# Kernel optimization log

Hardware: AMD Instinct MI355X
Metric: run time of the kernel (lower is better)

## Reference

```python
import jax, jax.numpy as jnp
import numpy as np

B, T, K, H = 32, 128, 16, 4   # batch, agents, in_dim, num_heads
A = 2                          # out_dim (action dim)
H1 = H2 = 256
LOG_STD_MIN, LOG_STD_MAX = -20.0, 2.0


def _linear_params(key, out_dim, in_dim, uniform_w=None):
    k1, k2 = jax.random.split(key)
    if uniform_w is not None:
        w = jax.random.uniform(k1, (out_dim, in_dim), minval=-uniform_w, maxval=uniform_w)
        b = jax.random.uniform(k2, (out_dim,), minval=-uniform_w, maxval=uniform_w)
    else:
        bound = 1.0 / np.sqrt(in_dim)
        w = jax.random.uniform(k1, (out_dim, in_dim), minval=-bound, maxval=bound)
        b = jax.random.uniform(k2, (out_dim,), minval=-bound, maxval=bound)
    return w.astype(jnp.float32), b.astype(jnp.float32)


def setup_inputs() -> dict:
    key = jax.random.key(0)
    ks = jax.random.split(key, 10)
    state = jax.random.normal(ks[0], (B, T, K), dtype=jnp.float32)
    eps = jax.random.normal(ks[1], (B, T, A), dtype=jnp.float32)
    Wq, bq = _linear_params(ks[2], K * H, K)
    Wk, bk = _linear_params(ks[3], K * H, K)
    Wv, bv = _linear_params(ks[4], K * H, K)
    W1, b1 = _linear_params(ks[5], H1, K * H + K)
    W2, b2 = _linear_params(ks[6], H2, H1)
    Wmu, bmu = _linear_params(ks[7], A, H2, uniform_w=0.003)
    Wls, bls = _linear_params(ks[8], A, H2, uniform_w=0.003)
    return {"state": state, "eps": eps, "Wq": Wq, "bq": bq, "Wk": Wk, "bk": bk,
            "Wv": Wv, "bv": bv, "W1": W1, "b1": b1, "W2": W2, "b2": b2,
            "Wmu": Wmu, "bmu": bmu, "Wls": Wls, "bls": bls}


def reference(state, eps, Wq, bq, Wk, bk, Wv, bv, W1, b1, W2, b2, Wmu, bmu, Wls, bls):
    b, t, k = state.shape
    h = H
    # rel[b,i,j] = state[b,j] - state[b,i]
    rel = state[:, None, :, :] - state[:, :, None, :]          # (b,t,t,k)
    q = jax.nn.relu(state @ Wq.T + bq).reshape(b, t, h, k)     # (b,t,h,k)
    q = q.transpose(0, 2, 1, 3)                                # (b,h,t,k)
    Kt = jax.nn.relu(rel @ Wk.T + bk).reshape(b, t, t, h, k)   # (b,i,j,h,k)
    V = jax.nn.relu(rel @ Wv.T + bv).reshape(b, t, t, h, k)
    # scores over pairwise keys vs per-agent query; softmax over j (dim=2 in torch)
    s = jnp.einsum('bijhk,bhik->bhij', Kt, q) / jnp.sqrt(jnp.float32(k))
    w = jax.nn.softmax(s, axis=3)                              # softmax over j
    x = jnp.einsum('bhij,bijhk->bhik', w, V)                   # (b,h,t,k)
    x = x.transpose(0, 2, 1, 3).reshape(b, t, h * k)           # (b,t,h*k)
    x = jnp.concatenate([x, state], axis=-1)                   # (b,t,h*k+k)
    x = jax.nn.relu(x @ W1.T + b1)
    x = jax.nn.relu(x @ W2.T + b2)
    mu = jnp.tanh(x @ Wmu.T + bmu)
    log_std = jnp.tanh(x @ Wls.T + bls)
    log_std = LOG_STD_MIN + 0.5 * (LOG_STD_MAX - LOG_STD_MIN) * (log_std + 1.0)
    std = jnp.exp(log_std)
    z = mu + std * eps                                         # rsample
    action = jnp.tanh(z)
    # Normal log_prob with (z-mu)/std == eps, minus tanh correction
    log_prob = (-0.5 * eps * eps - log_std - 0.5 * jnp.log(2.0 * jnp.pi)) \
               - jnp.log(1.0 - action * action + 1e-7)
    log_prob = jnp.sum(log_prob, axis=-1, keepdims=True)
    return action, log_prob
```

## Files before the change

### kernel.cpp

```cpp
#include <hip/hip_runtime.h>
#include <math.h>

#define NB 32
#define NT 128
#define KD 16

#define QG_OFF   0u
#define PKH_OFF  1048576u
#define PVT_OFF  1572864u
#define W1P_OFF  2097152u
#define W2P_OFF  2146304u

typedef float f32x4 __attribute__((ext_vector_type(4)));
typedef short bf16x8 __attribute__((ext_vector_type(8)));
typedef __fp16 f16x2 __attribute__((ext_vector_type(2)));
union U4B8 { uint4 u; bf16x8 h; };
union U4H8 { uint4 u; f16x2 h[4]; };

#define L_PK 0
#define L_PV 18432
#define L_P  35840
#define L_X  44544
#define L_TOT 47872
#define L_H1 0
#define L_H2 8448

__device__ __forceinline__ unsigned short bf16rne(float f) {
    unsigned u = __float_as_uint(f);
    return (unsigned short)((u + 0x7fffu + ((u >> 16) & 1u)) >> 16);
}
__device__ __forceinline__ void unpack8(uint4 u, float* f) {
    f[0] = __uint_as_float(u.x << 16); f[1] = __uint_as_float(u.x & 0xffff0000u);
    f[2] = __uint_as_float(u.y << 16); f[3] = __uint_as_float(u.y & 0xffff0000u);
    f[4] = __uint_as_float(u.z << 16); f[5] = __uint_as_float(u.z & 0xffff0000u);
    f[6] = __uint_as_float(u.w << 16); f[7] = __uint_as_float(u.w & 0xffff0000u);
}
__device__ __forceinline__ f16x2 pkmax(f16x2 a, f16x2 b) {
    f16x2 d;
    asm("v_pk_max_f16 %0, %1, %2" : "=v"(d) : "v"(a), "v"(b));
    return d;
}
#if __has_builtin(__builtin_amdgcn_fdot2)
#define FDOT2(a, b, c) __builtin_amdgcn_fdot2((a), (b), (c), false)
#else
#define FDOT2(a, b, c) ((c) + (float)(a)[0] * (float)(b)[0] + (float)(a)[1] * (float)(b)[1])
#endif

__global__ __launch_bounds__(256) void prep_kernel(
    const float* __restrict__ state,
    const float* __restrict__ Wq, const float* __restrict__ bq,
    const float* __restrict__ Wk, const float* __restrict__ Wv,
    const float* __restrict__ W1, const float* __restrict__ W2,
    char* __restrict__ wsb)
{
    const int blk = blockIdx.x, tid = threadIdx.x;
    float* Qg = (float*)(wsb + QG_OFF);
    unsigned short* PkH = (unsigned short*)(wsb + PKH_OFF);
    unsigned short* PvT = (unsigned short*)(wsb + PVT_OFF);

    if (blk < 128) {
        __shared__ float Wl[3][64][17];
        __shared__ float Sl[32][17];
        const int b = blk >> 2, r0 = (blk & 3) * 32;
        for (int idx = tid; idx < 1024; idx += 256) {
            int o = idx >> 4, m = idx & 15;
            Wl[0][o][m] = Wq[idx];
            Wl[1][o][m] = Wk[idx];
            Wl[2][o][m] = Wv[idx];
        }
        for (int idx = tid; idx < 512; idx += 256)
            Sl[idx >> 4][idx & 15] = state[(size_t)(b * NT + r0) * KD + idx];
        __syncthreads();
        const int o = tid & 63, rr = tid >> 6;
        float wqv[16], wkv[16], wvv[16];
        #pragma unroll
        for (int m = 0; m < 16; ++m) {
            wqv[m] = Wl[0][o][m]; wkv[m] = Wl[1][o][m]; wvv[m] = Wl[2][o][m];
        }
        const float bqo = bq[o];
        for (int r = rr; r < 32; r += 4) {
            float aq = bqo, ak = 0.f, av = 0.f;
            #pragma unroll
            for (int m = 0; m < 16; ++m) {
                float s = Sl[r][m];
                aq = fmaf(s, wqv[m], aq);
                ak = fmaf(s, wkv[m], ak);
                av = fmaf(s, wvv[m], av);
            }
            int row = b * NT + r0 + r;
            Qg[row * 64 + o] = fmaxf(aq, 0.f) * 0.25f;
            __fp16 hk = (__fp16)ak;
            PkH[(size_t)b * 8192 + (r0 + r) * 64 + o] = *(unsigned short*)&hk;
            __fp16 hv = (__fp16)av;
            PvT[(size_t)b * 8192 + o * NT + (r0 + r)] = *(unsigned short*)&hv;
        }
    } else if (blk < 140) {
        int fi = (blk - 128) * 256 + tid;
        int l = fi & 63, rest = fi >> 6;
        int t = rest & 15, ks = rest >> 4;
        int n = t * 16 + (l & 15);
        int kb = ks * 32 + (l >> 4) * 8;
        unsigned short v[8];
        #pragma unroll
        for (int j = 0; j < 8; ++j) {
            int k = kb + j;
            v[j] = (k < 80) ? bf16rne(W1[n * 80 + k]) : (unsigned short)0;
        }
        uint4 u;
        u.x = (unsigned)v[0] | ((unsigned)v[1] << 16);
        u.y = (unsigned)v[2] | ((unsigned)v[3] << 16);
        u.z = (unsigned)v[4] | ((unsigned)v[5] << 16);
        u.w = (unsigned)v[6] | ((unsigned)v[7] << 16);
        ((uint4*)(wsb + W1P_OFF))[fi] = u;
    } else {
        int fi = (blk - 140) * 256 + tid;
        int l = fi & 63, rest = fi >> 6;
        int t = rest & 15, ks = rest >> 4;
        int n = t * 16 + (l & 15);
        int kb = ks * 32 + (l >> 4) * 8;
        unsigned short v[8];
        #pragma unroll
        for (int j = 0; j < 8; ++j) v[j] = bf16rne(W2[n * 256 + kb + j]);
        uint4 u;
        u.x = (unsigned)v[0] | ((unsigned)v[1] << 16);
        u.y = (unsigned)v[2] | ((unsigned)v[3] << 16);
        u.z = (unsigned)v[4] | ((unsigned)v[5] << 16);
        u.w = (unsigned)v[6] | ((unsigned)v[7] << 16);
        ((uint4*)(wsb + W2P_OFF))[fi] = u;
    }
}

__global__ __launch_bounds__(512, 4) void actor_kernel(
    const float* __restrict__ state, const float* __restrict__ eps,
    const float* __restrict__ bkg, const float* __restrict__ bvg,
    const float* __restrict__ b1g, const float* __restrict__ b2g,
    const float* __restrict__ Wmu, const float* __restrict__ bmu,
    const float* __restrict__ Wls, const float* __restrict__ bls,
    const char* __restrict__ wsb, float* __restrict__ out)
{
    __shared__ __align__(16) char sm[L_TOT];

    const int tid = threadIdx.x, w = tid >> 6, lane = tid & 63;
    const int bid = blockIdx.x;
    const int b    = (bid & 7) * 4 + ((bid >> 3) >> 4);
    const int tile = (bid >> 3) & 15;
    const int iloc = tile * 8 + w;
    const int row  = b * NT + iloc;
    const int h = lane >> 4, s = lane & 15, h16 = h << 4;
    const int g = h, lr = s;
    const int t0 = 2 * w;
    const int n0 = w * 32 + lr, n1 = n0 + 16;

    const float* Qg = (const float*)(wsb + QG_OFF);

    {
        const uint4* srcK = (const uint4*)(wsb + PKH_OFF) + (size_t)b * 1024;
        #pragma unroll
        for (int it = 0; it < 2; ++it) {
            int idx = tid + it * 512;
            int r = idx >> 3, c = idx & 7;
            *(uint4*)(sm + L_PK + r * 144 + c * 16) = srcK[idx];
        }
        const uint4* srcV = (const uint4*)(wsb + PVT_OFF) + (size_t)b * 1024;
        #pragma unroll
        for (int it = 0; it < 2; ++it) {
            int idx = tid + it * 512;
            int o = idx >> 4, c = idx & 15;
            *(uint4*)(sm + L_PV + o * 272 + c * 16) = srcV[idx];
        }
        if (tid < 384) {
            int r = 8 + tid / 48, c2 = (tid % 48) * 2;
            *(unsigned*)((unsigned short*)(sm + L_X) + r * 104 + c2) = 0u;
        }
    }

    float qf[16], bkf[16];
    {
        const float4* qa  = (const float4*)(Qg + (size_t)row * 64 + h16);
        const float4* bk4 = (const float4*)(bkg + h16);
        #pragma unroll
        for (int q4 = 0; q4 < 4; ++q4) {
            float4 a = qa[q4], k4 = bk4[q4];
            qf[q4*4+0]=a.x; qf[q4*4+1]=a.y; qf[q4*4+2]=a.z; qf[q4*4+3]=a.w;
            bkf[q4*4+0]=k4.x; bkf[q4*4+1]=k4.y; bkf[q4*4+2]=k4.z; bkf[q4*4+3]=k4.w;
        }
    }
    const float bvo = bvg[lane];
    float stt = 0.f;
    if (tid < 128)
        stt = state[((size_t)b * NT + tile * 8 + (tid >> 4)) * KD + (tid & 15)];
    __syncthreads();

    f16x2 q8[8], mb8[8];
    float dotc;
    {
        U4H8 p0, p1;
        p0.u = *(const uint4*)(sm + L_PK + iloc * 144 + h * 32);
        p1.u = *(const uint4*)(sm + L_PK + iloc * 144 + h * 32 + 16);
        #pragma unroll
        for (int t = 0; t < 4; ++t) {
            q8[t]     = __builtin_amdgcn_cvt_pkrtz(qf[2*t],   qf[2*t+1]);
            q8[4 + t] = __builtin_amdgcn_cvt_pkrtz(qf[8+2*t], qf[8+2*t+1]);
            f16x2 b0 = __builtin_amdgcn_cvt_pkrtz(bkf[2*t],   bkf[2*t+1]);
            f16x2 b1 = __builtin_amdgcn_cvt_pkrtz(bkf[8+2*t], bkf[8+2*t+1]);
            mb8[t]     = p0.h[t] - b0;
            mb8[4 + t] = p1.h[t] - b1;
        }
        float d0 = 0.f, d1 = 0.f;
        #pragma unroll
        for (int t = 0; t < 4; ++t) {
            d0 = FDOT2(q8[t],     mb8[t],     d0);
            d1 = FDOT2(q8[4 + t], mb8[4 + t], d1);
        }
        dotc = -(d0 + d1);
    }

    float sc[8];
    #pragma unroll
    for (int jj = 0; jj < 8; ++jj) {
        const char* pr = sm + L_PK + (s + (jj << 4)) * 144 + h * 32;
        U4H8 v0, v1;
        v0.u = *(const uint4*)(pr);
        v1.u = *(const uint4*)(pr + 16);
        float aE = 0.f, aO = 0.f;
        #pragma unroll
        for (int t = 0; t < 4; ++t) {
            aE = FDOT2(q8[t],     pkmax(v0.h[t], mb8[t]),     aE);
            aO = FDOT2(q8[4 + t], pkmax(v1.h[t], mb8[4 + t]), aO);
        }
        sc[jj] = dotc + aE + aO;
    }

    float mx = sc[0];
    #pragma unroll
    for (int jj = 1; jj < 8; ++jj) mx = fmaxf(mx, sc[jj]);
    #pragma unroll
    for (int off = 1; off < 16; off <<= 1) mx = fmaxf(mx, __shfl_xor(mx, off));
    float l = 0.f;
    #pragma unroll
    for (int jj = 0; jj < 8; ++jj) { sc[jj] = __expf(sc[jj] - mx); l += sc[jj]; }
    #pragma unroll
    for (int off = 1; off < 16; off <<= 1) l += __shfl_xor(l, off);
    const float rl = 1.0f / l;
    {
        __fp16* prow = (__fp16*)(sm + L_P) + (w * 4 + h) * 136;
        #pragma unroll
        for (int jj = 0; jj < 8; ++jj) prow[(jj << 4) + s] = (__fp16)sc[jj];
    }
    asm volatile("s_waitcnt lgkmcnt(0)" ::: "memory");
    __builtin_amdgcn_sched_barrier(0);

    const uint4* W1P = (const uint4*)(wsb + W1P_OFF);
    uint4 w1f0[3], w1f1[3];
    #pragma unroll
    for (int ks = 0; ks < 3; ++ks) {
        w1f0[ks] = W1P[((ks << 4) + t0) * 64 + lane];
        w1f1[ks] = W1P[((ks << 4) + t0 + 1) * 64 + lane];
    }

    float xA;
    {
        const __fp16 pvi = *((const __fp16*)(sm + L_PV) + lane * 136 + iloc);
        const float mbvf = (float)pvi - bvo;
        const __fp16 mbvh = (__fp16)mbvf;
        const f16x2 mbv2 = {mbvh, mbvh};
        const uint4* vrow = (const uint4*)(sm + L_PV + lane * 272);
        const uint4* prow = (const uint4*)(sm + L_P + (w * 4 + h) * 272);
        float acc = 0.f;
        #pragma unroll
        for (int u = 0; u < 16; ++u) {
            U4H8 v; v.u = vrow[u];
            U4H8 p; p.u = prow[u];
            #pragma unroll
            for (int t = 0; t < 4; ++t)
                acc = FDOT2(p.h[t], pkmax(v.h[t], mbv2), acc);
        }
        xA = fmaf(rl, acc, -(float)mbvh);
    }

    ((unsigned short*)(sm + L_X))[w * 104 + lane] = bf16rne(xA);
    if (tid < 128) {
        unsigned short* xr = (unsigned short*)(sm + L_X) + (tid >> 4) * 104;
        xr[64 + (tid & 15)] = bf16rne(stt);
        xr[80 + (tid & 15)] = 0;
    }
    __syncthreads();

    const uint4* W2P = (const uint4*)(wsb + W2P_OFF);
    uint4 w2f0[4], w2f1[4];
    #pragma unroll
    for (int ks = 0; ks < 4; ++ks) {
        w2f0[ks] = W2P[((ks << 4) + t0) * 64 + lane];
        w2f1[ks] = W2P[((ks << 4) + t0 + 1) * 64 + lane];
    }
    {
        f32x4 a0 = {0.f, 0.f, 0.f, 0.f}, a1 = a0;
        #pragma unroll
        for (int ks = 0; ks < 3; ++ks) {
            U4B8 av; av.u = *(const uint4*)(sm + L_X + (lr * 104 + ks * 32 + g * 8) * 2);
            U4B8 b0; b0.u = w1f0[ks];
            U4B8 b1; b1.u = w1f1[ks];
            a0 = __builtin_amdgcn_mfma_f32_16x16x32_bf16(av.h, b0.h, a0, 0, 0, 0);
            a1 = __builtin_amdgcn_mfma_f32_16x16x32_bf16(av.h, b1.h, a1, 0, 0, 0);
        }
        const float bn0 = b1g[n0], bn1 = b1g[n1];
        #pragma unroll
        for (int qq = 0; qq < 4; ++qq) {
            *((unsigned short*)(sm + L_H1) + (4 * g + qq) * 264 + n0) =
                bf16rne(fmaxf(a0[qq] + bn0, 0.f));
            *((unsigned short*)(sm + L_H1) + (4 * g + qq) * 264 + n1) =
                bf16rne(fmaxf(a1[qq] + bn1, 0.f));
        }
    }
    __syncthreads();

    {
        f32x4 a0 = {0.f, 0.f, 0.f, 0.f}, a1 = a0;
        #pragma unroll
        for (int ks = 0; ks < 4; ++ks) {
            U4B8 av; av.u = *(const uint4*)(sm + L_H1 + (lr * 264 + ks * 32 + g * 8) * 2);
            U4B8 b0; b0.u = w2f0[ks];
            U4B8 b1; b1.u = w2f1[ks];
            a0 = __builtin_amdgcn_mfma_f32_16x16x32_bf16(av.h, b0.h, a0, 0, 0, 0);
            a1 = __builtin_amdgcn_mfma_f32_16x16x32_bf16(av.h, b1.h, a1, 0, 0, 0);
        }
        #pragma unroll
        for (int ks = 4; ks < 8; ++ks) {
            U4B8 av; av.u = *(const uint4*)(sm + L_H1 + (lr * 264 + ks * 32 + g * 8) * 2);
            U4B8 b0; b0.u = W2P[((ks << 4) + t0) * 64 + lane];
            U4B8 b1; b1.u = W2P[((ks << 4) + t0 + 1) * 64 + lane];
            a0 = __builtin_amdgcn_mfma_f32_16x16x32_bf16(av.h, b0.h, a0, 0, 0, 0);
            a1 = __builtin_amdgcn_mfma_f32_16x16x32_bf16(av.h, b1.h, a1, 0, 0, 0);
        }
        const float bn0 = b2g[n0], bn1 = b2g[n1];
        #pragma unroll
        for (int qq = 0; qq < 4; ++qq) {
            *((unsigned short*)(sm + L_H2) + (4 * g + qq) * 264 + n0) =
                bf16rne(fmaxf(a0[qq] + bn0, 0.f));
            *((unsigned short*)(sm + L_H2) + (4 * g + qq) * 264 + n1) =
                bf16rne(fmaxf(a1[qq] + bn1, 0.f));
        }
    }
    __syncthreads();

    {
        const int g2 = tid >> 4, m = g2 >> 2, d = g2 & 3, cc = tid & 15;
        const float* wrow = (d < 2) ? (Wmu + d * 256) : (Wls + (d - 2) * 256);
        float hbuf[16];
        uint4 ha = *(const uint4*)(sm + L_H2 + (m * 264 + cc * 16) * 2);
        uint4 hb = *(const uint4*)(sm + L_H2 + (m * 264 + cc * 16 + 8) * 2);
        unpack8(ha, hbuf); unpack8(hb, hbuf + 8);
        float dd = 0.f;
        #pragma unroll
        for (int kk = 0; kk < 16; ++kk)
            dd = fmaf(hbuf[kk], wrow[cc * 16 + kk], dd);
        #pragma unroll
        for (int off = 1; off < 16; off <<= 1) dd += __shfl_xor(dd, off);
        float* hd = (float*)(sm + L_P);
        if (cc == 0) {
            float bias = (d < 2) ? bmu[d] : bls[d - 2];
            hd[m * 4 + d] = tanhf(dd + bias);
        }
    }
    __syncthreads();
    if (tid < 8) {
        const float* hd = (const float*)(sm + L_P);
        const int m = tid;
        const int orow = b * NT + tile * 8 + m;
        float lp = 0.f;
        #pragma unroll
        for (int d = 0; d < 2; ++d) {
            float mu  = hd[m * 4 + d];
            float lsr = hd[m * 4 + 2 + d];
            float ls  = -20.f + 11.f * (lsr + 1.f);
            float e   = eps[orow * 2 + d];
            float z   = mu + __expf(ls) * e;
            float a   = tanhf(z);
            out[orow * 2 + d] = a;
            lp += -0.5f * e * e - ls - 0.91893853320467274f - __logf(1.f - a * a + 1e-7f);
        }
        out[NB * NT * 2 + orow] = lp;
    }
}

extern "C" void kernel_launch(void* const* d_in, const int* in_sizes, int n_in,
                              void* d_out, int out_size, void* d_ws, size_t ws_size,
                              hipStream_t stream) {
    const float* state = (const float*)d_in[0];
    const float* eps   = (const float*)d_in[1];
    const float* Wq    = (const float*)d_in[2];
    const float* bq    = (const float*)d_in[3];
    const float* Wk    = (const float*)d_in[4];
    const float* bk    = (const float*)d_in[5];
    const float* Wv    = (const float*)d_in[6];
    const float* bv    = (const float*)d_in[7];
    const float* W1    = (const float*)d_in[8];
    const float* b1    = (const float*)d_in[9];
    const float* W2    = (const float*)d_in[10];
    const float* b2    = (const float*)d_in[11];
    const float* Wmu   = (const float*)d_in[12];
    const float* bmu   = (const float*)d_in[13];
    const float* Wls   = (const float*)d_in[14];
    const float* bls   = (const float*)d_in[15];
    float* out = (float*)d_out;
    char* wsb  = (char*)d_ws;

    prep_kernel<<<172, 256, 0, stream>>>(state, Wq, bq, Wk, Wv, W1, W2, wsb);
    actor_kernel<<<512, 512, 0, stream>>>(state, eps, bk, bv, b1, b2,
                                          Wmu, bmu, Wls, bls, wsb, out);
}
```

Baseline: 21.40 us.

## Fuse Q/K/V projection into actor kernel, dropping global workspace round-trip

```diff
diff --git a/kernel.cpp b/kernel.cpp
--- a/kernel.cpp
+++ b/kernel.cpp
@@ -5,11 +5,8 @@
 #define NT 128
 #define KD 16
 
-#define QG_OFF   0u
-#define PKH_OFF  1048576u
-#define PVT_OFF  1572864u
-#define W1P_OFF  2097152u
-#define W2P_OFF  2146304u
+#define W1P_OFF 0u
+#define W2P_OFF 49152u
 
 typedef float f32x4 __attribute__((ext_vector_type(4)));
 typedef short bf16x8 __attribute__((ext_vector_type(8)));
@@ -17,17 +14,22 @@
 union U4B8 { uint4 u; bf16x8 h; };
 union U4H8 { uint4 u; f16x2 h[4]; };
 
-#define L_PK 0
-#define L_PV 18432
-#define L_P  35840
-#define L_X  44544
-#define L_TOT 47872
-#define L_H1 0
-#define L_H2 8448
+#define L_S  0
+#define L_X  0
+#define L_PK 8704
+#define L_PV 27136
+#define L_P  44544
+#define L_TOT 53248
+#define L_H1 8704
+#define L_H2 17152
 
 __device__ __forceinline__ unsigned short bf16rne(float f) {
     unsigned u = __float_as_uint(f);
     return (unsigned short)((u + 0x7fffu + ((u >> 16) & 1u)) >> 16);
+}
+__device__ __forceinline__ unsigned cvt2h(float a, float b) {
+    f16x2 t = __builtin_amdgcn_cvt_pkrtz(a, b);
+    return *(unsigned*)&t;
 }
 __device__ __forceinline__ void unpack8(uint4 u, float* f) {
     f[0] = __uint_as_float(u.x << 16); f[1] = __uint_as_float(u.x & 0xffff0000u);
@@ -47,55 +49,12 @@
 #endif
 
 __global__ __launch_bounds__(256) void prep_kernel(
-    const float* __restrict__ state,
-    const float* __restrict__ Wq, const float* __restrict__ bq,
-    const float* __restrict__ Wk, const float* __restrict__ Wv,
     const float* __restrict__ W1, const float* __restrict__ W2,
     char* __restrict__ wsb)
 {
     const int blk = blockIdx.x, tid = threadIdx.x;
-    float* Qg = (float*)(wsb + QG_OFF);
-    unsigned short* PkH = (unsigned short*)(wsb + PKH_OFF);
-    unsigned short* PvT = (unsigned short*)(wsb + PVT_OFF);
-
-    if (blk < 128) {
-        __shared__ float Wl[3][64][17];
-        __shared__ float Sl[32][17];
-        const int b = blk >> 2, r0 = (blk & 3) * 32;
-        for (int idx = tid; idx < 1024; idx += 256) {
-            int o = idx >> 4, m = idx & 15;
-            Wl[0][o][m] = Wq[idx];
-            Wl[1][o][m] = Wk[idx];
-            Wl[2][o][m] = Wv[idx];
-        }
-        for (int idx = tid; idx < 512; idx += 256)
-            Sl[idx >> 4][idx & 15] = state[(size_t)(b * NT + r0) * KD + idx];
-        __syncthreads();
-        const int o = tid & 63, rr = tid >> 6;
-        float wqv[16], wkv[16], wvv[16];
-        #pragma unroll
-        for (int m = 0; m < 16; ++m) {
-            wqv[m] = Wl[0][o][m]; wkv[m] = Wl[1][o][m]; wvv[m] = Wl[2][o][m];
-        }
-        const float bqo = bq[o];
-        for (int r = rr; r < 32; r += 4) {
-            float aq = bqo, ak = 0.f, av = 0.f;
-            #pragma unroll
-            for (int m = 0; m < 16; ++m) {
-                float s = Sl[r][m];
-                aq = fmaf(s, wqv[m], aq);
-                ak = fmaf(s, wkv[m], ak);
-                av = fmaf(s, wvv[m], av);
-            }
-            int row = b * NT + r0 + r;
-            Qg[row * 64 + o] = fmaxf(aq, 0.f) * 0.25f;
-            __fp16 hk = (__fp16)ak;
-            PkH[(size_t)b * 8192 + (r0 + r) * 64 + o] = *(unsigned short*)&hk;
-            __fp16 hv = (__fp16)av;
-            PvT[(size_t)b * 8192 + o * NT + (r0 + r)] = *(unsigned short*)&hv;
-        }
-    } else if (blk < 140) {
-        int fi = (blk - 128) * 256 + tid;
+    if (blk < 12) {
+        int fi = blk * 256 + tid;
         int l = fi & 63, rest = fi >> 6;
         int t = rest & 15, ks = rest >> 4;
         int n = t * 16 + (l & 15);
@@ -113,7 +72,7 @@
         u.w = (unsigned)v[6] | ((unsigned)v[7] << 16);
         ((uint4*)(wsb + W1P_OFF))[fi] = u;
     } else {
-        int fi = (blk - 140) * 256 + tid;
+        int fi = (blk - 12) * 256 + tid;
         int l = fi & 63, rest = fi >> 6;
         int t = rest & 15, ks = rest >> 4;
         int n = t * 16 + (l & 15);
@@ -130,79 +89,117 @@
     }
 }
 
-__global__ __launch_bounds__(512, 4) void actor_kernel(
+__global__ __launch_bounds__(512, 6) void actor_kernel(
     const float* __restrict__ state, const float* __restrict__ eps,
-    const float* __restrict__ bkg, const float* __restrict__ bvg,
+    const float* __restrict__ Wq, const float* __restrict__ bq,
+    const float* __restrict__ Wk, const float* __restrict__ bkg,
+    const float* __restrict__ Wv, const float* __restrict__ bvg,
     const float* __restrict__ b1g, const float* __restrict__ b2g,
     const float* __restrict__ Wmu, const float* __restrict__ bmu,
     const float* __restrict__ Wls, const float* __restrict__ bls,
     const char* __restrict__ wsb, float* __restrict__ out)
 {
     __shared__ __align__(16) char sm[L_TOT];
+    float* smS = (float*)(sm + L_S);
 
     const int tid = threadIdx.x, w = tid >> 6, lane = tid & 63;
     const int bid = blockIdx.x;
-    const int b    = (bid & 7) * 4 + ((bid >> 3) >> 4);
+    const int b    = (bid & 7) * 4 + (bid >> 7);
     const int tile = (bid >> 3) & 15;
     const int iloc = tile * 8 + w;
-    const int row  = b * NT + iloc;
-    const int h = lane >> 4, s = lane & 15, h16 = h << 4;
+    const int h = lane >> 4, s = lane & 15;
     const int g = h, lr = s;
     const int t0 = 2 * w;
     const int n0 = w * 32 + lr, n1 = n0 + 16;
 
-    const float* Qg = (const float*)(wsb + QG_OFF);
-
-    {
-        const uint4* srcK = (const uint4*)(wsb + PKH_OFF) + (size_t)b * 1024;
-        #pragma unroll
-        for (int it = 0; it < 2; ++it) {
-            int idx = tid + it * 512;
-            int r = idx >> 3, c = idx & 7;
-            *(uint4*)(sm + L_PK + r * 144 + c * 16) = srcK[idx];
-        }
-        const uint4* srcV = (const uint4*)(wsb + PVT_OFF) + (size_t)b * 1024;
-        #pragma unroll
-        for (int it = 0; it < 2; ++it) {
-            int idx = tid + it * 512;
-            int o = idx >> 4, c = idx & 15;
-            *(uint4*)(sm + L_PV + o * 272 + c * 16) = srcV[idx];
-        }
-        if (tid < 384) {
-            int r = 8 + tid / 48, c2 = (tid % 48) * 2;
-            *(unsigned*)((unsigned short*)(sm + L_X) + r * 104 + c2) = 0u;
-        }
-    }
-
-    float qf[16], bkf[16];
-    {
-        const float4* qa  = (const float4*)(Qg + (size_t)row * 64 + h16);
-        const float4* bk4 = (const float4*)(bkg + h16);
-        #pragma unroll
-        for (int q4 = 0; q4 < 4; ++q4) {
-            float4 a = qa[q4], k4 = bk4[q4];
-            qf[q4*4+0]=a.x; qf[q4*4+1]=a.y; qf[q4*4+2]=a.z; qf[q4*4+3]=a.w;
-            bkf[q4*4+0]=k4.x; bkf[q4*4+1]=k4.y; bkf[q4*4+2]=k4.z; bkf[q4*4+3]=k4.w;
-        }
-    }
-    const float bvo = bvg[lane];
+    {
+        float4 v = ((const float4*)(state + (size_t)b * NT * KD))[tid];
+        int r = tid >> 2, c = (tid & 3) * 4;
+        float* dst = smS + r * 17 + c;
+        dst[0] = v.x; dst[1] = v.y; dst[2] = v.z; dst[3] = v.w;
+    }
+    float wqv[16], wkv[16], wvv[16];
+    {
+        const float4* q4 = (const float4*)(Wq + lane * KD);
+        const float4* k4 = (const float4*)(Wk + lane * KD);
+        const float4* v4 = (const float4*)(Wv + lane * KD);
+        #pragma unroll
+        for (int r4 = 0; r4 < 4; ++r4) {
+            float4 a = q4[r4], c = k4[r4], d = v4[r4];
+            wqv[r4*4+0]=a.x; wqv[r4*4+1]=a.y; wqv[r4*4+2]=a.z; wqv[r4*4+3]=a.w;
+            wkv[r4*4+0]=c.x; wkv[r4*4+1]=c.y; wkv[r4*4+2]=c.z; wkv[r4*4+3]=c.w;
+            wvv[r4*4+0]=d.x; wvv[r4*4+1]=d.y; wvv[r4*4+2]=d.z; wvv[r4*4+3]=d.w;
+        }
+    }
+    const float bqo = bq[lane], bvo = bvg[lane];
     float stt = 0.f;
     if (tid < 128)
         stt = state[((size_t)b * NT + tile * 8 + (tid >> 4)) * KD + (tid & 15)];
     __syncthreads();
 
+    float qo;
+    {
+        const float* sr = smS + iloc * 17;
+        float aq = bqo;
+        #pragma unroll
+        for (int m = 0; m < 16; ++m) aq = fmaf(sr[m], wqv[m], aq);
+        qo = fmaxf(aq, 0.f) * 0.25f;
+    }
+    {
+        const int oe = lane & ~1;
+        #pragma unroll
+        for (int p = 0; p < 8; ++p) {
+            int r0 = w * 16 + 2 * p;
+            const float* s0 = smS + r0 * 17;
+            const float* s1 = s0 + 17;
+            float ak0 = 0.f, av0 = 0.f, ak1 = 0.f, av1 = 0.f;
+            #pragma unroll
+            for (int m = 0; m < 16; ++m) {
+                float w_k = wkv[m], w_v = wvv[m];
+                ak0 = fmaf(s0[m], w_k, ak0);
+                av0 = fmaf(s0[m], w_v, av0);
+                ak1 = fmaf(s1[m], w_k, ak1);
+                av1 = fmaf(s1[m], w_v, av1);
+            }
+            float pk0 = __shfl_xor(ak0, 1);
+            float pk1 = __shfl_xor(ak1, 1);
+            unsigned val = (lane & 1) ? cvt2h(pk1, ak1) : cvt2h(ak0, pk0);
+            int rowk = r0 + (lane & 1);
+            *(unsigned*)(sm + L_PK + rowk * 144 + oe * 2) = val;
+            *(unsigned*)(sm + L_PV + lane * 272 + r0 * 2) = cvt2h(av0, av1);
+        }
+    }
+    __syncthreads();
+
+    if (tid < 384) {
+        int r = 8 + tid / 48, c2 = (tid % 48) * 2;
+        *(unsigned*)((unsigned short*)(sm + L_X) + r * 104 + c2) = 0u;
+    }
+
     f16x2 q8[8], mb8[8];
     float dotc;
     {
+        const int h16 = h << 4;
+        float bkf[16];
+        {
+            const float4* bk4 = (const float4*)(bkg + h16);
+            #pragma unroll
+            for (int q4 = 0; q4 < 4; ++q4) {
+                float4 k4 = bk4[q4];
+                bkf[q4*4+0]=k4.x; bkf[q4*4+1]=k4.y; bkf[q4*4+2]=k4.z; bkf[q4*4+3]=k4.w;
+            }
+        }
         U4H8 p0, p1;
         p0.u = *(const uint4*)(sm + L_PK + iloc * 144 + h * 32);
         p1.u = *(const uint4*)(sm + L_PK + iloc * 144 + h * 32 + 16);
         #pragma unroll
         for (int t = 0; t < 4; ++t) {
-            q8[t]     = __builtin_amdgcn_cvt_pkrtz(qf[2*t],   qf[2*t+1]);
-            q8[4 + t] = __builtin_amdgcn_cvt_pkrtz(qf[8+2*t], qf[8+2*t+1]);
+            float qa0 = __shfl(qo, h16 + 2*t),     qb0 = __shfl(qo, h16 + 2*t + 1);
+            float qa1 = __shfl(qo, h16 + 8 + 2*t), qb1 = __shfl(qo, h16 + 9 + 2*t);
+            q8[t]     = __builtin_amdgcn_cvt_pkrtz(qa0, qb0);
+            q8[4 + t] = __builtin_amdgcn_cvt_pkrtz(qa1, qb1);
             f16x2 b0 = __builtin_amdgcn_cvt_pkrtz(bkf[2*t],   bkf[2*t+1]);
-            f16x2 b1 = __builtin_amdgcn_cvt_pkrtz(bkf[8+2*t], bkf[8+2*t+1]);
+            f16x2 b1 = __builtin_amdgcn_cvt_pkrtz(bkf[8+2*t], bkf[9+2*t]);
             mb8[t]     = p0.h[t] - b0;
             mb8[4 + t] = p1.h[t] - b1;
         }
@@ -287,9 +284,9 @@
     __syncthreads();
 
     const uint4* W2P = (const uint4*)(wsb + W2P_OFF);
-    uint4 w2f0[4], w2f1[4];
-    #pragma unroll
-    for (int ks = 0; ks < 4; ++ks) {
+    uint4 w2f0[2], w2f1[2];
+    #pragma unroll
+    for (int ks = 0; ks < 2; ++ks) {
         w2f0[ks] = W2P[((ks << 4) + t0) * 64 + lane];
         w2f1[ks] = W2P[((ks << 4) + t0 + 1) * 64 + lane];
     }
@@ -317,7 +314,7 @@
     {
         f32x4 a0 = {0.f, 0.f, 0.f, 0.f}, a1 = a0;
         #pragma unroll
-        for (int ks = 0; ks < 4; ++ks) {
+        for (int ks = 0; ks < 2; ++ks) {
             U4B8 av; av.u = *(const uint4*)(sm + L_H1 + (lr * 264 + ks * 32 + g * 8) * 2);
             U4B8 b0; b0.u = w2f0[ks];
             U4B8 b1; b1.u = w2f1[ks];
@@ -325,7 +322,7 @@
             a1 = __builtin_amdgcn_mfma_f32_16x16x32_bf16(av.h, b1.h, a1, 0, 0, 0);
         }
         #pragma unroll
-        for (int ks = 4; ks < 8; ++ks) {
+        for (int ks = 2; ks < 8; ++ks) {
             U4B8 av; av.u = *(const uint4*)(sm + L_H1 + (lr * 264 + ks * 32 + g * 8) * 2);
             U4B8 b0; b0.u = W2P[((ks << 4) + t0) * 64 + lane];
             U4B8 b1; b1.u = W2P[((ks << 4) + t0 + 1) * 64 + lane];
@@ -405,7 +402,7 @@
     float* out = (float*)d_out;
     char* wsb  = (char*)d_ws;
 
-    prep_kernel<<<172, 256, 0, stream>>>(state, Wq, bq, Wk, Wv, W1, W2, wsb);
-    actor_kernel<<<512, 512, 0, stream>>>(state, eps, bk, bv, b1, b2,
-                                          Wmu, bmu, Wls, bls, wsb, out);
-}
+    prep_kernel<<<44, 256, 0, stream>>>(W1, W2, wsb);
+    actor_kernel<<<512, 512, 0, stream>>>(state, eps, Wq, bq, Wk, bk, Wv, bv,
+                                          b1, b2, Wmu, bmu, Wls, bls, wsb, out);
+}
```

After: 26.75 us. +25.0%, slower.

## Halve agents per block, split heads across warp pairs, double grid

Applied to the files above, without the earlier changes.

```diff
diff --git a/kernel.cpp b/kernel.cpp
--- a/kernel.cpp
+++ b/kernel.cpp
@@ -18,10 +18,10 @@
 union U4H8 { uint4 u; f16x2 h[4]; };
 
 #define L_PK 0
-#define L_PV 18432
-#define L_P  35840
-#define L_X  44544
-#define L_TOT 47872
+#define L_PV 16896
+#define L_P  34048
+#define L_X  38336
+#define L_TOT 41664
 #define L_H1 0
 #define L_H2 8448
 
@@ -130,7 +130,7 @@
     }
 }
 
-__global__ __launch_bounds__(512, 4) void actor_kernel(
+__global__ __launch_bounds__(512, 6) void actor_kernel(
     const float* __restrict__ state, const float* __restrict__ eps,
     const float* __restrict__ bkg, const float* __restrict__ bvg,
     const float* __restrict__ b1g, const float* __restrict__ b2g,
@@ -142,12 +142,15 @@
 
     const int tid = threadIdx.x, w = tid >> 6, lane = tid & 63;
     const int bid = blockIdx.x;
-    const int b    = (bid & 7) * 4 + ((bid >> 3) >> 4);
-    const int tile = (bid >> 3) & 15;
-    const int iloc = tile * 8 + w;
+    const int x = bid & 7, y = bid >> 3;
+    const int b    = x * 4 + (y >> 5);
+    const int tile = y & 31;
+    const int r  = w >> 1, hh = w & 1;
+    const int iloc = tile * 4 + r;
     const int row  = b * NT + iloc;
-    const int h = lane >> 4, s = lane & 15, h16 = h << 4;
-    const int g = h, lr = s;
+    const int hl = lane >> 5, s = lane & 31;
+    const int h  = 2 * hh + hl, h16 = h << 4;
+    const int g = lane >> 4 & 3, lr = lane & 15;
     const int t0 = 2 * w;
     const int n0 = w * 32 + lr, n1 = n0 + 16;
 
@@ -158,19 +161,19 @@
         #pragma unroll
         for (int it = 0; it < 2; ++it) {
             int idx = tid + it * 512;
-            int r = idx >> 3, c = idx & 7;
-            *(uint4*)(sm + L_PK + r * 144 + c * 16) = srcK[idx];
+            int rr = idx >> 3, c = idx & 7;
+            *(uint4*)(sm + L_PK + rr * 132 + c * 16) = srcK[idx];
         }
         const uint4* srcV = (const uint4*)(wsb + PVT_OFF) + (size_t)b * 1024;
         #pragma unroll
         for (int it = 0; it < 2; ++it) {
             int idx = tid + it * 512;
             int o = idx >> 4, c = idx & 15;
-            *(uint4*)(sm + L_PV + o * 272 + c * 16) = srcV[idx];
-        }
-        if (tid < 384) {
-            int r = 8 + tid / 48, c2 = (tid % 48) * 2;
-            *(unsigned*)((unsigned short*)(sm + L_X) + r * 104 + c2) = 0u;
+            *(uint4*)(sm + L_PV + o * 268 + c * 16) = srcV[idx];
+        }
+        for (int idx = tid; idx < 576; idx += 512) {
+            int rr = 4 + idx / 48, c2 = (idx % 48) * 2;
+            *(unsigned*)((unsigned short*)(sm + L_X) + rr * 104 + c2) = 0u;
         }
     }
 
@@ -185,18 +188,17 @@
             bkf[q4*4+0]=k4.x; bkf[q4*4+1]=k4.y; bkf[q4*4+2]=k4.z; bkf[q4*4+3]=k4.w;
         }
     }
-    const float bvo = bvg[lane];
     float stt = 0.f;
-    if (tid < 128)
-        stt = state[((size_t)b * NT + tile * 8 + (tid >> 4)) * KD + (tid & 15)];
+    if (tid < 64)
+        stt = state[((size_t)b * NT + tile * 4 + (tid >> 4)) * KD + (tid & 15)];
     __syncthreads();
 
     f16x2 q8[8], mb8[8];
     float dotc;
     {
         U4H8 p0, p1;
-        p0.u = *(const uint4*)(sm + L_PK + iloc * 144 + h * 32);
-        p1.u = *(const uint4*)(sm + L_PK + iloc * 144 + h * 32 + 16);
+        p0.u = *(const uint4*)(sm + L_PK + iloc * 132 + h * 32);
+        p1.u = *(const uint4*)(sm + L_PK + iloc * 132 + h * 32 + 16);
         #pragma unroll
         for (int t = 0; t < 4; ++t) {
             q8[t]     = __builtin_amdgcn_cvt_pkrtz(qf[2*t],   qf[2*t+1]);
@@ -215,10 +217,10 @@
         dotc = -(d0 + d1);
     }
 
-    float sc[8];
-    #pragma unroll
-    for (int jj = 0; jj < 8; ++jj) {
-        const char* pr = sm + L_PK + (s + (jj << 4)) * 144 + h * 32;
+    float sc[4];
+    #pragma unroll
+    for (int jj = 0; jj < 4; ++jj) {
+        const char* pr = sm + L_PK + (s + (jj << 5)) * 132 + h * 32;
         U4H8 v0, v1;
         v0.u = *(const uint4*)(pr);
         v1.u = *(const uint4*)(pr + 16);
@@ -231,21 +233,19 @@
         sc[jj] = dotc + aE + aO;
     }
 
-    float mx = sc[0];
-    #pragma unroll
-    for (int jj = 1; jj < 8; ++jj) mx = fmaxf(mx, sc[jj]);
-    #pragma unroll
-    for (int off = 1; off < 16; off <<= 1) mx = fmaxf(mx, __shfl_xor(mx, off));
+    float mx = fmaxf(fmaxf(sc[0], sc[1]), fmaxf(sc[2], sc[3]));
+    #pragma unroll
+    for (int off = 1; off < 32; off <<= 1) mx = fmaxf(mx, __shfl_xor(mx, off));
     float l = 0.f;
     #pragma unroll
-    for (int jj = 0; jj < 8; ++jj) { sc[jj] = __expf(sc[jj] - mx); l += sc[jj]; }
-    #pragma unroll
-    for (int off = 1; off < 16; off <<= 1) l += __shfl_xor(l, off);
+    for (int jj = 0; jj < 4; ++jj) { sc[jj] = __expf(sc[jj] - mx); l += sc[jj]; }
+    #pragma unroll
+    for (int off = 1; off < 32; off <<= 1) l += __shfl_xor(l, off);
     const float rl = 1.0f / l;
     {
-        __fp16* prow = (__fp16*)(sm + L_P) + (w * 4 + h) * 136;
-        #pragma unroll
-        for (int jj = 0; jj < 8; ++jj) prow[(jj << 4) + s] = (__fp16)sc[jj];
+        __fp16* prow = (__fp16*)(sm + L_P) + (r * 4 + h) * 134;
+        #pragma unroll
+        for (int jj = 0; jj < 4; ++jj) prow[(jj << 5) + s] = (__fp16)sc[jj];
     }
     asm volatile("s_waitcnt lgkmcnt(0)" ::: "memory");
     __builtin_amdgcn_sched_barrier(0);
@@ -258,28 +258,33 @@
         w1f1[ks] = W1P[((ks << 4) + t0 + 1) * 64 + lane];
     }
 
-    float xA;
-    {
-        const __fp16 pvi = *((const __fp16*)(sm + L_PV) + lane * 136 + iloc);
-        const float mbvf = (float)pvi - bvo;
+    {
+        const int jh = lane >> 5, op = lane & 31;
+        const int o = 32 * hh + op;
+        const int ho = 2 * hh + (op >> 4);
+        const __fp16 pvi = *((const __fp16*)(sm + L_PV) + o * 134 + iloc);
+        const float mbvf = (float)pvi - bvg[o];
         const __fp16 mbvh = (__fp16)mbvf;
         const f16x2 mbv2 = {mbvh, mbvh};
-        const uint4* vrow = (const uint4*)(sm + L_PV + lane * 272);
-        const uint4* prow = (const uint4*)(sm + L_P + (w * 4 + h) * 272);
+        const uint4* vrow = (const uint4*)(sm + L_PV + o * 268 + jh * 128);
+        const uint4* prow = (const uint4*)(sm + L_P + (r * 4 + ho) * 268 + jh * 128);
         float acc = 0.f;
         #pragma unroll
-        for (int u = 0; u < 16; ++u) {
+        for (int u = 0; u < 8; ++u) {
             U4H8 v; v.u = vrow[u];
             U4H8 p; p.u = prow[u];
             #pragma unroll
             for (int t = 0; t < 4; ++t)
                 acc = FDOT2(p.h[t], pkmax(v.h[t], mbv2), acc);
         }
-        xA = fmaf(rl, acc, -(float)mbvh);
-    }
-
-    ((unsigned short*)(sm + L_X))[w * 104 + lane] = bf16rne(xA);
-    if (tid < 128) {
+        acc += __shfl_xor(acc, 32);
+        if (jh == 0) {
+            float xA = fmaf(rl * 0.f + rl, acc, 0.f);
+            xA = fmaf(rl, acc, -(float)mbvh);
+            ((unsigned short*)(sm + L_X))[r * 104 + o] = bf16rne(xA);
+        }
+    }
+    if (tid < 64) {
         unsigned short* xr = (unsigned short*)(sm + L_X) + (tid >> 4) * 104;
         xr[64 + (tid & 15)] = bf16rne(stt);
         xr[80 + (tid & 15)] = 0;
@@ -287,9 +292,9 @@
     __syncthreads();
 
     const uint4* W2P = (const uint4*)(wsb + W2P_OFF);
-    uint4 w2f0[4], w2f1[4];
-    #pragma unroll
-    for (int ks = 0; ks < 4; ++ks) {
+    uint4 w2f0[2], w2f1[2];
+    #pragma unroll
+    for (int ks = 0; ks < 2; ++ks) {
         w2f0[ks] = W2P[((ks << 4) + t0) * 64 + lane];
         w2f1[ks] = W2P[((ks << 4) + t0 + 1) * 64 + lane];
     }
@@ -317,7 +322,7 @@
     {
         f32x4 a0 = {0.f, 0.f, 0.f, 0.f}, a1 = a0;
         #pragma unroll
-        for (int ks = 0; ks < 4; ++ks) {
+        for (int ks = 0; ks < 2; ++ks) {
             U4B8 av; av.u = *(const uint4*)(sm + L_H1 + (lr * 264 + ks * 32 + g * 8) * 2);
             U4B8 b0; b0.u = w2f0[ks];
             U4B8 b1; b1.u = w2f1[ks];
@@ -325,7 +330,7 @@
             a1 = __builtin_amdgcn_mfma_f32_16x16x32_bf16(av.h, b1.h, a1, 0, 0, 0);
         }
         #pragma unroll
-        for (int ks = 4; ks < 8; ++ks) {
+        for (int ks = 2; ks < 8; ++ks) {
             U4B8 av; av.u = *(const uint4*)(sm + L_H1 + (lr * 264 + ks * 32 + g * 8) * 2);
             U4B8 b0; b0.u = W2P[((ks << 4) + t0) * 64 + lane];
             U4B8 b1; b1.u = W2P[((ks << 4) + t0 + 1) * 64 + lane];
@@ -343,7 +348,7 @@
     }
     __syncthreads();
 
-    {
+    if (tid < 256) {
         const int g2 = tid >> 4, m = g2 >> 2, d = g2 & 3, cc = tid & 15;
         const float* wrow = (d < 2) ? (Wmu + d * 256) : (Wls + (d - 2) * 256);
         float hbuf[16];
@@ -363,10 +368,10 @@
         }
     }
     __syncthreads();
-    if (tid < 8) {
+    if (tid < 4) {
         const float* hd = (const float*)(sm + L_P);
         const int m = tid;
-        const int orow = b * NT + tile * 8 + m;
+        const int orow = b * NT + tile * 4 + m;
         float lp = 0.f;
         #pragma unroll
         for (int d = 0; d < 2; ++d) {
@@ -406,6 +411,6 @@
     char* wsb  = (char*)d_ws;
 
     prep_kernel<<<172, 256, 0, stream>>>(state, Wq, bq, Wk, Wv, W1, W2, wsb);
-    actor_kernel<<<512, 512, 0, stream>>>(state, eps, bk, bv, b1, b2,
-                                          Wmu, bmu, Wls, bls, wsb, out);
-}
+    actor_kernel<<<1024, 512, 0, stream>>>(state, eps, bk, bv, b1, b2,
+                                           Wmu, bmu, Wls, bls, wsb, out);
+}
```

Result: slower. 45.47 us (+112.5%).

## Store Q as fp16 and read V rows directly from global instead of LDS

Applied to the files above, without the earlier changes.

```diff
diff --git a/kernel.cpp b/kernel.cpp
--- a/kernel.cpp
+++ b/kernel.cpp
@@ -5,11 +5,11 @@
 #define NT 128
 #define KD 16
 
-#define QG_OFF   0u
-#define PKH_OFF  1048576u
-#define PVT_OFF  1572864u
-#define W1P_OFF  2097152u
-#define W2P_OFF  2146304u
+#define QH_OFF   0u
+#define PKH_OFF  524288u
+#define PVT_OFF  1048576u
+#define W1P_OFF  1572864u
+#define W2P_OFF  1622016u
 
 typedef float f32x4 __attribute__((ext_vector_type(4)));
 typedef short bf16x8 __attribute__((ext_vector_type(8)));
@@ -18,10 +18,9 @@
 union U4H8 { uint4 u; f16x2 h[4]; };
 
 #define L_PK 0
-#define L_PV 18432
-#define L_P  35840
-#define L_X  44544
-#define L_TOT 47872
+#define L_P  18432
+#define L_X  27136
+#define L_TOT 30464
 #define L_H1 0
 #define L_H2 8448
 
@@ -54,7 +53,7 @@
     char* __restrict__ wsb)
 {
     const int blk = blockIdx.x, tid = threadIdx.x;
-    float* Qg = (float*)(wsb + QG_OFF);
+    unsigned short* QH  = (unsigned short*)(wsb + QH_OFF);
     unsigned short* PkH = (unsigned short*)(wsb + PKH_OFF);
     unsigned short* PvT = (unsigned short*)(wsb + PVT_OFF);
 
@@ -88,7 +87,8 @@
                 av = fmaf(s, wvv[m], av);
             }
             int row = b * NT + r0 + r;
-            Qg[row * 64 + o] = fmaxf(aq, 0.f) * 0.25f;
+            __fp16 hq = (__fp16)(fmaxf(aq, 0.f) * 0.25f);
+            QH[row * 64 + o] = *(unsigned short*)&hq;
             __fp16 hk = (__fp16)ak;
             PkH[(size_t)b * 8192 + (r0 + r) * 64 + o] = *(unsigned short*)&hk;
             __fp16 hv = (__fp16)av;
@@ -146,12 +146,13 @@
     const int tile = (bid >> 3) & 15;
     const int iloc = tile * 8 + w;
     const int row  = b * NT + iloc;
-    const int h = lane >> 4, s = lane & 15, h16 = h << 4;
+    const int h = lane >> 4, s = lane & 15;
     const int g = h, lr = s;
     const int t0 = 2 * w;
     const int n0 = w * 32 + lr, n1 = n0 + 16;
 
-    const float* Qg = (const float*)(wsb + QG_OFF);
+    const unsigned short* QH  = (const unsigned short*)(wsb + QH_OFF);
+    const __fp16* PvH = (const __fp16*)(wsb + PVT_OFF);
 
     {
         const uint4* srcK = (const uint4*)(wsb + PKH_OFF) + (size_t)b * 1024;
@@ -161,27 +162,21 @@
             int r = idx >> 3, c = idx & 7;
             *(uint4*)(sm + L_PK + r * 144 + c * 16) = srcK[idx];
         }
-        const uint4* srcV = (const uint4*)(wsb + PVT_OFF) + (size_t)b * 1024;
-        #pragma unroll
-        for (int it = 0; it < 2; ++it) {
-            int idx = tid + it * 512;
-            int o = idx >> 4, c = idx & 15;
-            *(uint4*)(sm + L_PV + o * 272 + c * 16) = srcV[idx];
-        }
         if (tid < 384) {
             int r = 8 + tid / 48, c2 = (tid % 48) * 2;
             *(unsigned*)((unsigned short*)(sm + L_X) + r * 104 + c2) = 0u;
         }
     }
 
-    float qf[16], bkf[16];
-    {
-        const float4* qa  = (const float4*)(Qg + (size_t)row * 64 + h16);
-        const float4* bk4 = (const float4*)(bkg + h16);
+    U4H8 qh0, qh1;
+    qh0.u = *(const uint4*)(QH + (size_t)row * 64 + (h << 4));
+    qh1.u = *(const uint4*)(QH + (size_t)row * 64 + (h << 4) + 8);
+    float bkf[16];
+    {
+        const float4* bk4 = (const float4*)(bkg + (h << 4));
         #pragma unroll
         for (int q4 = 0; q4 < 4; ++q4) {
-            float4 a = qa[q4], k4 = bk4[q4];
-            qf[q4*4+0]=a.x; qf[q4*4+1]=a.y; qf[q4*4+2]=a.z; qf[q4*4+3]=a.w;
+            float4 k4 = bk4[q4];
             bkf[q4*4+0]=k4.x; bkf[q4*4+1]=k4.y; bkf[q4*4+2]=k4.z; bkf[q4*4+3]=k4.w;
         }
     }
@@ -199,8 +194,8 @@
         p1.u = *(const uint4*)(sm + L_PK + iloc * 144 + h * 32 + 16);
         #pragma unroll
         for (int t = 0; t < 4; ++t) {
-            q8[t]     = __builtin_amdgcn_cvt_pkrtz(qf[2*t],   qf[2*t+1]);
-            q8[4 + t] = __builtin_amdgcn_cvt_pkrtz(qf[8+2*t], qf[8+2*t+1]);
+            q8[t]     = qh0.h[t];
+            q8[4 + t] = qh1.h[t];
             f16x2 b0 = __builtin_amdgcn_cvt_pkrtz(bkf[2*t],   bkf[2*t+1]);
             f16x2 b1 = __builtin_amdgcn_cvt_pkrtz(bkf[8+2*t], bkf[8+2*t+1]);
             mb8[t]     = p0.h[t] - b0;
@@ -260,11 +255,11 @@
 
     float xA;
     {
-        const __fp16 pvi = *((const __fp16*)(sm + L_PV) + lane * 136 + iloc);
+        const __fp16 pvi = PvH[(size_t)b * 8192 + lane * NT + iloc];
         const float mbvf = (float)pvi - bvo;
         const __fp16 mbvh = (__fp16)mbvf;
         const f16x2 mbv2 = {mbvh, mbvh};
-        const uint4* vrow = (const uint4*)(sm + L_PV + lane * 272);
+        const uint4* vrow = (const uint4*)(PvH + (size_t)b * 8192 + lane * NT);
         const uint4* prow = (const uint4*)(sm + L_P + (w * 4 + h) * 272);
         float acc = 0.f;
         #pragma unroll
```

Result: slower. 26.77 us (+25.1%).
